# Kernel optimization log

Measured on AMD Instinct MI355X. Metric: run time of the kernel, lower is better.

The kernel has to match this reference:

```python
import jax, jax.numpy as jnp
import numpy as np

NUM_CLASSES = 80
SCORE_TH = 0.5
NMS_TH = 0.3
TOPK = 100          # per-class candidates kept before NMS
MAX_PER_IMAGE = 100
ANCHOR_MASK = [[6, 7, 8], [3, 4, 5], [0, 1, 2]]


def _decode_layer(f, anch, image_shape, input_shape):
    # f: [B, A*(5+C), gh, gw] -> boxes [B, gh*gw*A, 4], scores [B, gh*gw*A, C]
    B, _, gh, gw = f.shape
    A = anch.shape[0]
    f = f.reshape(B, A, NUM_CLASSES + 5, gh, gw).transpose(0, 3, 4, 1, 2)  # [B,gh,gw,A,5+C]
    gx = jnp.arange(gw, dtype=f.dtype)
    gy = jnp.arange(gh, dtype=f.dtype)
    X, Y = jnp.meshgrid(gx, gy, indexing='xy')            # each [gh,gw]
    grid = jnp.stack([X, Y], -1)[None, :, :, None, :]     # [1,gh,gw,1,2] (x,y)
    # faithful to original: divide (x,y) by tensor([gh,gw])
    box_xy = (jax.nn.sigmoid(f[..., :2]) + grid) / jnp.array([gh, gw], f.dtype)
    box_wh = jnp.exp(f[..., 2:4]) * anch[None, None, None, :, :] / input_shape
    conf = jax.nn.sigmoid(f[..., 4:5])
    probs = jax.nn.sigmoid(f[..., 5:])
    # yolo_correct_boxes (letterbox undo in normalized coords)
    box_yx = box_xy[..., ::-1]
    box_hw = box_wh[..., ::-1]
    new_shape = jnp.round(image_shape * jnp.min(input_shape / image_shape))
    offset = (input_shape - new_shape) / 2.0 / input_shape
    scale = input_shape / new_shape
    box_yx = (box_yx - offset) * scale
    box_hw = box_hw * scale
    mins = box_yx - box_hw / 2.0
    maxes = box_yx + box_hw / 2.0
    boxes = jnp.concatenate([mins, maxes], -1) * jnp.concatenate([image_shape, image_shape])
    return boxes.reshape(B, -1, 4), (conf * probs).reshape(B, -1, NUM_CLASSES)


def _pairwise_iou(b):  # b: [K,4] corner boxes
    area = jnp.maximum(b[:, 2] - b[:, 0], 0.0) * jnp.maximum(b[:, 3] - b[:, 1], 0.0)
    tl = jnp.maximum(b[:, None, :2], b[None, :, :2])
    br = jnp.minimum(b[:, None, 2:4], b[None, :, 2:4])
    wh = jnp.maximum(br - tl, 0.0)
    inter = wh[..., 0] * wh[..., 1]
    return inter / (area[:, None] + area[None, :] - inter + 1e-9)


def _detect(feats0, feats1, feats2, anchors, image_shape, ori_shape):
    input_shape = jnp.array([feats0.shape[2] * 32, feats0.shape[3] * 32], feats0.dtype)
    boxes_l, scores_l = [], []
    for l, f in enumerate([feats0, feats1, feats2]):
        b, s = _decode_layer(f, anchors[jnp.array(ANCHOR_MASK[l])], image_shape, input_shape)
        boxes_l.append(b)
        scores_l.append(s)
    boxes = jnp.concatenate(boxes_l, axis=1)    # [B,N,4]
    scores = jnp.concatenate(scores_l, axis=1)  # [B,N,C]

    def per_image(boxes_i, scores_i, ori_i):
        def per_class(sc):  # sc: [N]
            sc_m = jnp.where(sc >= SCORE_TH, sc, -1.0)
            vals, idx = jax.lax.top_k(sc_m, TOPK)      # sorted desc, like torch.sort
            b = boxes_i[idx]                            # [K,4]
            valid = vals >= SCORE_TH
            iou = _pairwise_iou(b)
            rng = jnp.arange(TOPK)
            def body(i, keep):
                sup = (iou[i] > NMS_TH) & (rng > i) & keep[i]
                return keep & ~sup
            keep = jax.lax.fori_loop(0, TOPK, body, valid)
            return b, vals, keep

        cand_b, cand_s, keep = jax.vmap(per_class, in_axes=1)(scores_i)  # [C,K,...]
        flat_s = jnp.where(keep, cand_s, -1.0).reshape(-1)               # [C*K]
        vals2, idx2 = jax.lax.top_k(flat_s, MAX_PER_IMAGE)
        det_boxes = cand_b.reshape(-1, 4)[idx2]                          # [M,4]
        det_valid = vals2 >= SCORE_TH
        det_cls = (idx2 // TOPK + 1).astype(jnp.int32)                   # classes shifted by +1
        # undo letterbox back to original image coords (per yolo_eval tail)
        w, h = image_shape[0], image_shape[1]
        iw, ih = ori_i[0], ori_i[1]
        scale = jnp.minimum(w / iw, h / ih)
        nw = jnp.floor(iw * scale)
        nh = jnp.floor(ih * scale)
        dx = jnp.floor((w - nw) / 2.0)
        dy = jnp.floor((h - nh) / 2.0)
        b02 = (det_boxes[:, jnp.array([0, 2])] - dx) / scale
        b13 = (det_boxes[:, jnp.array([1, 3])] - dy) / scale
        resc = jnp.stack([b02[:, 0], b13[:, 0], b02[:, 1], b13[:, 1]], -1)
        dets = jnp.concatenate([resc, vals2[:, None]], -1)               # [M,5]
        dets = jnp.where(det_valid[:, None], dets, 0.0)
        det_cls = jnp.where(det_valid, det_cls, 0)
        return dets, det_cls, det_valid

    return jax.vmap(per_image)(boxes, scores, ori_shape)


def setup_inputs() -> dict:
    key = jax.random.key(0)
    k0, k1, k2, k3 = jax.random.split(key, 4)
    B = 8
    feats0 = jax.random.normal(k0, (B, 255, 19, 19), jnp.float32)
    feats1 = jax.random.normal(k1, (B, 255, 38, 38), jnp.float32)
    feats2 = jax.random.normal(k2, (B, 255, 76, 76), jnp.float32)
    anchors = jnp.array([[10, 13], [16, 30], [33, 23], [30, 61], [62, 45],
                         [59, 119], [116, 90], [156, 198], [373, 326]], jnp.float32)
    image_shape = jnp.array([608.0, 608.0], jnp.float32)
    ori_shape = jax.random.randint(k3, (B, 2), 480, 1280).astype(jnp.float32)
    return {"feats0": feats0, "feats1": feats1, "feats2": feats2,
            "anchors": anchors, "image_shape": image_shape, "ori_shape": ori_shape}


def reference(feats0, feats1, feats2, anchors, image_shape, ori_shape):
    # Returns padded detections: dets [B,100,5] (ymin,xmin,ymax,xmax,score),
    # classes [B,100] int32 (0 = padding), valid [B,100] bool.
    return _detect(feats0, feats1, feats2, anchors, image_shape, ori_shape)
```

## Files before the change

kernel.cpp:

```cpp
#include <hip/hip_runtime.h>
#include <hip/hip_bf16.h>


#define BATCH 8
#define NC 80
#define G0 19
#define G1 38
#define G2 76
#define C0 (G0*G0)
#define C1 (G1*G1)
#define C2 (G2*G2)
#define CELLS (C0+C1+C2)
#define PCELLS 7616
#define OFF_L0 0
#define OFF_L1 (C0*3)
#define OFF_L2 (OFF_L1 + C1*3)
#define NBOX (CELLS*3)
#define TK 100
#define SCORE_TH 0.5f
#define NMS_TH 0.3f

#define CPG 10
#define NCG (NC/CPG)
#define SBLK 448
#define CHUNKS (PCELLS/SBLK)
#define SUBS 8
#define CAPS 512
#define CAP (SUBS*CAPS)

#define OFF_CAND   ((size_t)0)
#define OFF_BOXES  ((size_t)20971520)
#define OFF_CSCORE ((size_t)23882624)
#define OFF_CBOX   ((size_t)24138624)
#define OFF_STAGE  ((size_t)25162624)
#define OFF_CNT    ((size_t)25226624)

__device__ __forceinline__ float sigmoidf_(float x) {
    return 1.0f / (1.0f + expf(-x));
}

__device__ __forceinline__ void bitonic_desc(unsigned long long* s, unsigned M,
                                             unsigned tid, unsigned nthr) {
    for (unsigned k = 2; k <= M; k <<= 1) {
        for (unsigned j = k >> 1; j > 0; j >>= 1) {
            for (unsigned t = tid; t < M; t += nthr) {
                unsigned p = t ^ j;
                if (p > t) {
                    unsigned long long a = s[t], b = s[p];
                    bool desc = ((t & k) == 0);
                    if (desc ? (a < b) : (a > b)) { s[t] = b; s[p] = a; }
                }
            }
            __syncthreads();
        }
    }
}

__device__ __forceinline__ void cell_decomp(int cell, int& g, int& cl, int& off, int& layer) {
    if (cell < C0)            { layer = 0; g = G0; cl = cell;            off = OFF_L0; }
    else if (cell < C0 + C1)  { layer = 1; g = G1; cl = cell - C0;       off = OFF_L1; }
    else                      { layer = 2; g = G2; cl = cell - C0 - C1;  off = OFF_L2; }
}

__global__ __launch_bounds__(256) void box_kernel(
        const float* __restrict__ f0, const float* __restrict__ f1,
        const float* __restrict__ f2, const float* __restrict__ anchors,
        const float* __restrict__ image_shape,
        float* __restrict__ boxes) {
    int t = blockIdx.x * blockDim.x + threadIdx.x;
    if (t >= BATCH * NBOX) return;
    int b = t / NBOX;
    int r = t - b * NBOX;
    int a = r % 3;
    int cell = r / 3;

    int layer, g, cl, off;
    cell_decomp(cell, g, cl, off, layer);
    const float* f;
    if (layer == 0)      f = f0 + (size_t)b * 255 * C0;
    else if (layer == 1) f = f1 + (size_t)b * 255 * C1;
    else                 f = f2 + (size_t)b * 255 * C2;
    int S = g * g;
    int y = cl / g;
    int x = cl - y * g;

    const float in0 = (float)(G0 * 32);
    const float in1 = (float)(G0 * 32);
    float img0 = image_shape[0], img1 = image_shape[1];
    float mr   = fminf(in0 / img0, in1 / img1);
    float new0 = rintf(img0 * mr), new1 = rintf(img1 * mr);
    float ofs0 = (in0 - new0) * 0.5f / in0;
    float ofs1 = (in1 - new1) * 0.5f / in1;
    float scl0 = in0 / new0, scl1 = in1 / new1;

    const float* fa = f + (size_t)(a * 85) * S + cl;
    float tx = fa[0];
    float ty = fa[(size_t)S];
    float tw = fa[(size_t)2 * S];
    float th = fa[(size_t)3 * S];

    int am = (2 - layer) * 3 + a;
    float aw = anchors[am * 2 + 0];
    float ah = anchors[am * 2 + 1];

    float bx = (sigmoidf_(tx) + (float)x) / (float)g;
    float by = (sigmoidf_(ty) + (float)y) / (float)g;
    float bw = expf(tw) * aw / in0;
    float bh = expf(th) * ah / in1;

    float yy = (by - ofs0) * scl0;
    float xx = (bx - ofs1) * scl1;
    float hh = bh * scl0;
    float ww = bw * scl1;

    float4 bb;
    bb.x = (yy - hh * 0.5f) * img0;
    bb.y = (xx - ww * 0.5f) * img1;
    bb.z = (yy + hh * 0.5f) * img0;
    bb.w = (xx + ww * 0.5f) * img1;

    *(float4*)(boxes + ((size_t)b * NBOX + r) * 4) = bb;
}

__global__ __launch_bounds__(SBLK) void score_kernel(
        const float* __restrict__ f0, const float* __restrict__ f1,
        const float* __restrict__ f2,
        unsigned* __restrict__ cnt,
        unsigned long long* __restrict__ cand) {
    int chunk = blockIdx.x;
    int pg = blockIdx.y;
    int cgrp = pg % NCG;
    int a    = (pg / NCG) % 3;
    int b    = pg / (NCG * 3);

    int cellp = chunk * SBLK + threadIdx.x;
    int sub = (chunk * 7 + (threadIdx.x >> 6)) & (SUBS - 1);
    bool vc = (cellp < CELLS);
    int cell = vc ? cellp : 0;

    int layer, g, cl, off;
    cell_decomp(cell, g, cl, off, layer);
    const float* f;
    if (layer == 0)      f = f0 + (size_t)b * 255 * C0;
    else if (layer == 1) f = f1 + (size_t)b * 255 * C1;
    else                 f = f2 + (size_t)b * 255 * C2;
    int S = g * g;
    const float* fa = f + (size_t)(a * 85) * S + cl;

    float tc = vc ? fa[(size_t)4 * S] : -1e30f;
    float conf = sigmoidf_(tc);
    int gidx = off + cl * 3 + a;
    int lane = threadIdx.x & 63;

    float pl[CPG];
    #pragma unroll
    for (int k = 0; k < CPG; ++k) {
        int c = cgrp * CPG + k;
        pl[k] = vc ? fa[(size_t)(5 + c) * S] : -1e30f;
    }

    float sc[CPG];
    bool pred[CPG];
    #pragma unroll
    for (int k = 0; k < CPG; ++k) {
        sc[k] = conf * sigmoidf_(pl[k]);
        pred[k] = vc && (sc[k] >= SCORE_TH);
    }

    #pragma unroll
    for (int k = 0; k < CPG; ++k) {
        unsigned long long m = __ballot(pred[k]);
        if (m) {
            int c = cgrp * CPG + k;
            int idx = (b * NC + c) * SUBS + sub;
            int leader = __ffsll((long long)m) - 1;
            unsigned base = 0;
            if (lane == leader) base = atomicAdd(&cnt[idx], (unsigned)__popcll(m));
            base = (unsigned)__shfl((int)base, leader);
            if (pred[k]) {
                unsigned rank = (unsigned)__popcll(m & ((1ULL << lane) - 1ULL));
                unsigned slot = base + rank;
                if (slot < CAPS) {
                    unsigned long long key =
                        ((unsigned long long)__float_as_uint(sc[k]) << 32) |
                        (unsigned)(~(unsigned)gidx);
                    cand[(size_t)idx * CAPS + slot] = key;
                }
            }
        }
    }
}

__global__ __launch_bounds__(512) void nms_kernel(
        const unsigned* __restrict__ cnt,
        const unsigned long long* __restrict__ cand,
        const float* __restrict__ boxes,
        float* __restrict__ cscore, float* __restrict__ cbox) {
    __shared__ unsigned long long s[CAP];
    __shared__ float bx[TK][4];
    __shared__ float sc[TK];
    __shared__ int keep[TK];

    int bc = blockIdx.x;
    int b = bc / NC;
    unsigned tid = threadIdx.x;

    unsigned nI[SUBS];
    unsigned pref[SUBS + 1];
    pref[0] = 0;
    #pragma unroll
    for (int i = 0; i < SUBS; ++i) {
        unsigned v = cnt[bc * SUBS + i];
        nI[i] = v > CAPS ? CAPS : v;
        pref[i + 1] = pref[i] + nI[i];
    }
    unsigned n = pref[SUBS];
    unsigned M = 128;
    while (M < n) M <<= 1;

    for (unsigned t = tid; t < M; t += 512) s[t] = 0ULL;
    __syncthreads();
    #pragma unroll
    for (int i = 0; i < SUBS; ++i) {
        const unsigned long long* cp = cand + (size_t)(bc * SUBS + i) * CAPS;
        for (unsigned t = tid; t < nI[i]; t += 512) s[pref[i] + t] = cp[t];
    }
    __syncthreads();

    bitonic_desc(s, M, tid, 512);

    int nv = (int)n < TK ? (int)n : TK;
    if (tid < TK) {
        if ((int)tid < nv) {
            unsigned long long key = s[tid];
            sc[tid] = __uint_as_float((unsigned)(key >> 32));
            unsigned gidx = ~(unsigned)(key & 0xFFFFFFFFu);
            const float* bp = boxes + ((size_t)b * NBOX + gidx) * 4;
            bx[tid][0] = bp[0]; bx[tid][1] = bp[1];
            bx[tid][2] = bp[2]; bx[tid][3] = bp[3];
            keep[tid] = 1;
        } else {
            sc[tid] = -1.0f;
            bx[tid][0] = bx[tid][1] = bx[tid][2] = bx[tid][3] = 0.0f;
            keep[tid] = 0;
        }
    }
    __syncthreads();

    for (int i = 0; i < nv - 1; ++i) {
        bool ki = (keep[i] != 0);
        if (ki && (int)tid > i && (int)tid < nv && keep[tid]) {
            float a0 = bx[i][0], a1 = bx[i][1], a2 = bx[i][2], a3 = bx[i][3];
            float c0 = bx[tid][0], c1 = bx[tid][1], c2 = bx[tid][2], c3 = bx[tid][3];
            float areaA = fmaxf(a2 - a0, 0.0f) * fmaxf(a3 - a1, 0.0f);
            float areaC = fmaxf(c2 - c0, 0.0f) * fmaxf(c3 - c1, 0.0f);
            float tl0 = fmaxf(a0, c0), tl1 = fmaxf(a1, c1);
            float br0 = fminf(a2, c2), br1 = fminf(a3, c3);
            float w = fmaxf(br0 - tl0, 0.0f), h = fmaxf(br1 - tl1, 0.0f);
            float inter = w * h;
            float iou = inter / (areaA + areaC - inter + 1e-9f);
            if (iou > NMS_TH) keep[tid] = 0;
        }
        __syncthreads();
    }

    if (tid < TK) {
        int c = bc - b * NC;
        size_t o = (size_t)b * 8000 + (size_t)c * TK + tid;
        bool k = (keep[tid] != 0);
        cscore[o] = k ? sc[tid] : -1.0f;
        float* cb = cbox + o * 4;
        cb[0] = bx[tid][0]; cb[1] = bx[tid][1];
        cb[2] = bx[tid][2]; cb[3] = bx[tid][3];
    }
}

__device__ __forceinline__ unsigned fflip(float v) {
    unsigned u = __float_as_uint(v);
    return (u & 0x80000000u) ? ~u : (u | 0x80000000u);
}
__device__ __forceinline__ float funflip(unsigned u) {
    return __uint_as_float((u & 0x80000000u) ? (u & 0x7FFFFFFFu) : ~u);
}

__global__ __launch_bounds__(256) void topk1_kernel(
        const float* __restrict__ cscore, unsigned long long* __restrict__ stage) {
    __shared__ unsigned long long s[1024];
    int blk = blockIdx.x;
    int b = blk / 10;
    int g = blk - b * 10;
    unsigned tid = threadIdx.x;
    for (unsigned t = tid; t < 1024; t += 256) {
        unsigned long long key = 0ULL;
        if (t < 800) {
            unsigned e = (unsigned)(g * 800 + t);
            float v = cscore[(size_t)b * 8000 + e];
            key = ((unsigned long long)fflip(v) << 32) | (unsigned)(~e);
        }
        s[t] = key;
    }
    __syncthreads();
    bitonic_desc(s, 1024, tid, 256);
    if (tid < TK) stage[(size_t)b * 1000 + (size_t)g * TK + tid] = s[tid];
}

__global__ __launch_bounds__(256) void topk2_kernel(
        const unsigned long long* __restrict__ stage,
        const float* __restrict__ cbox,
        const float* __restrict__ image_shape,
        const float* __restrict__ ori,
        float* __restrict__ out) {
    __shared__ unsigned long long s[1024];
    int b = blockIdx.x;
    unsigned tid = threadIdx.x;
    for (unsigned t = tid; t < 1024; t += 256)
        s[t] = (t < 1000) ? stage[(size_t)b * 1000 + t] : 0ULL;
    __syncthreads();
    bitonic_desc(s, 1024, tid, 256);

    if (tid < TK) {
        unsigned long long key = s[tid];
        float v = funflip((unsigned)(key >> 32));
        unsigned e = ~(unsigned)(key & 0xFFFFFFFFu);
        bool valid = (v >= SCORE_TH);

        float w = image_shape[0], h = image_shape[1];
        float iw = ori[b * 2 + 0], ih = ori[b * 2 + 1];
        float scale = fminf(w / iw, h / ih);
        float nw = floorf(iw * scale), nh = floorf(ih * scale);
        float dx = floorf((w - nw) * 0.5f), dy = floorf((h - nh) * 0.5f);

        const float* cb = cbox + ((size_t)b * 8000 + e) * 4;
        float r0 = (cb[0] - dx) / scale;
        float r1 = (cb[1] - dy) / scale;
        float r2 = (cb[2] - dx) / scale;
        float r3 = (cb[3] - dy) / scale;

        size_t row = (size_t)b * TK + tid;
        float* dp = out + row * 5;
        dp[0] = valid ? r0 : 0.0f;
        dp[1] = valid ? r1 : 0.0f;
        dp[2] = valid ? r2 : 0.0f;
        dp[3] = valid ? r3 : 0.0f;
        dp[4] = valid ? v  : 0.0f;
        out[(size_t)BATCH * TK * 5 + row] = valid ? (float)(e / TK + 1) : 0.0f;
        out[(size_t)BATCH * TK * 6 + row] = valid ? 1.0f : 0.0f;
    }
}

extern "C" void kernel_launch(void* const* d_in, const int* in_sizes, int n_in,
                              void* d_out, int out_size, void* d_ws, size_t ws_size,
                              hipStream_t stream) {
    const float* f0  = (const float*)d_in[0];
    const float* f1  = (const float*)d_in[1];
    const float* f2  = (const float*)d_in[2];
    const float* anc = (const float*)d_in[3];
    const float* ish = (const float*)d_in[4];
    const float* ori = (const float*)d_in[5];
    float* out = (float*)d_out;

    char* ws = (char*)d_ws;
    unsigned long long* cand  = (unsigned long long*)(ws + OFF_CAND);
    float*              boxes = (float*)(ws + OFF_BOXES);
    float*              cscr  = (float*)(ws + OFF_CSCORE);
    float*              cbox  = (float*)(ws + OFF_CBOX);
    unsigned long long* stage = (unsigned long long*)(ws + OFF_STAGE);
    unsigned*           cnt   = (unsigned*)(ws + OFF_CNT);

    hipMemsetAsync(cnt, 0, BATCH * NC * SUBS * sizeof(unsigned), stream);

    {
        int nThreads = BATCH * NBOX;
        int nBlocks = (nThreads + 255) / 256;
        box_kernel<<<nBlocks, 256, 0, stream>>>(f0, f1, f2, anc, ish, boxes);
    }

    {
        dim3 grid(CHUNKS, BATCH * 3 * NCG);
        score_kernel<<<grid, SBLK, 0, stream>>>(f0, f1, f2, cnt, cand);
    }

    nms_kernel<<<BATCH * NC, 512, 0, stream>>>(cnt, cand, boxes, cscr, cbox);

    topk1_kernel<<<BATCH * 10, 256, 0, stream>>>(cscr, stage);

    topk2_kernel<<<BATCH, 256, 0, stream>>>(stage, cbox, ish, ori, out);
}
```

Baseline: 331.8 us.

## Replace shared-memory bitonic sort and NMS with wavefront-shuffle top-k merge and NMS

The per-class NMS kernel now sorts 128-element chunks inside each wavefront with shuffle-based bitonic networks, then merges chunks pairwise keeping only the top 128, instead of a full block-wide bitonic sort with a barrier per step. The greedy NMS loop runs in a single wavefront, holding boxes and keep bits in registers and broadcasting by shuffle, which removes the per-iteration __syncthreads. It also uses float4 box loads and stores and halves the block size. The risks are extra shuffle instructions for 64-bit keys and a serial NMS loop on one wavefront while the other waves sit idle.

```diff
diff --git a/kernel.cpp b/kernel.cpp
--- a/kernel.cpp
+++ b/kernel.cpp
@@ -60,6 +60,56 @@
     if (cell < C0)            { layer = 0; g = G0; cl = cell;            off = OFF_L0; }
     else if (cell < C0 + C1)  { layer = 1; g = G1; cl = cell - C0;       off = OFF_L1; }
     else                      { layer = 2; g = G2; cl = cell - C0 - C1;  off = OFF_L2; }
+}
+
+__device__ __forceinline__ unsigned long long maxu(unsigned long long a, unsigned long long b) { return a > b ? a : b; }
+__device__ __forceinline__ unsigned long long minu(unsigned long long a, unsigned long long b) { return a < b ? a : b; }
+
+__device__ __forceinline__ unsigned long long ux64(unsigned long long v, int m) {
+    int lo = __shfl_xor((int)(unsigned)v, m, 64);
+    int hi = __shfl_xor((int)(unsigned)(v >> 32), m, 64);
+    return ((unsigned long long)(unsigned)hi << 32) | (unsigned)lo;
+}
+
+__device__ __forceinline__ void wsort128(unsigned long long& v0, unsigned long long& v1, int lane) {
+    #pragma unroll
+    for (int k = 2; k <= 32; k <<= 1) {
+        #pragma unroll
+        for (int j = k >> 1; j >= 1; j >>= 1) {
+            bool desc = ((lane & k) == 0);
+            bool lower = ((lane & j) == 0);
+            bool km = (lower == desc);
+            unsigned long long p0 = ux64(v0, j); v0 = km ? maxu(v0, p0) : minu(v0, p0);
+            unsigned long long p1 = ux64(v1, j); v1 = km ? maxu(v1, p1) : minu(v1, p1);
+        }
+    }
+    #pragma unroll
+    for (int j = 32; j >= 1; j >>= 1) {
+        bool lower = ((lane & j) == 0);
+        unsigned long long p0 = ux64(v0, j); v0 = lower ? maxu(v0, p0) : minu(v0, p0);
+        unsigned long long p1 = ux64(v1, j); v1 = lower ? minu(v1, p1) : maxu(v1, p1);
+    }
+    { unsigned long long t0 = maxu(v0, v1), t1 = minu(v0, v1); v0 = t0; v1 = t1; }
+    #pragma unroll
+    for (int j = 32; j >= 1; j >>= 1) {
+        bool lower = ((lane & j) == 0);
+        unsigned long long p0 = ux64(v0, j); v0 = lower ? maxu(v0, p0) : minu(v0, p0);
+        unsigned long long p1 = ux64(v1, j); v1 = lower ? maxu(v1, p1) : minu(v1, p1);
+    }
+}
+
+__device__ __forceinline__ void wmergetop(unsigned long long& a0, unsigned long long& a1,
+                                          unsigned long long b0, unsigned long long b1, int lane) {
+    unsigned long long r0 = ux64(b1, 63);
+    unsigned long long r1 = ux64(b0, 63);
+    a0 = maxu(a0, r0); a1 = maxu(a1, r1);
+    { unsigned long long t0 = maxu(a0, a1), t1 = minu(a0, a1); a0 = t0; a1 = t1; }
+    #pragma unroll
+    for (int j = 32; j >= 1; j >>= 1) {
+        bool lower = ((lane & j) == 0);
+        unsigned long long p0 = ux64(a0, j); a0 = lower ? maxu(a0, p0) : minu(a0, p0);
+        unsigned long long p1 = ux64(a1, j); a1 = lower ? maxu(a1, p1) : minu(a1, p1);
+    }
 }
 
 __global__ __launch_bounds__(256) void box_kernel(
@@ -191,87 +241,120 @@
     }
 }
 
-__global__ __launch_bounds__(512) void nms_kernel(
+__global__ __launch_bounds__(256) void nms_kernel(
         const unsigned* __restrict__ cnt,
         const unsigned long long* __restrict__ cand,
         const float* __restrict__ boxes,
         float* __restrict__ cscore, float* __restrict__ cbox) {
-    __shared__ unsigned long long s[CAP];
-    __shared__ float bx[TK][4];
-    __shared__ float sc[TK];
-    __shared__ int keep[TK];
+    __shared__ unsigned long long s[SUBS * CAPS];
 
     int bc = blockIdx.x;
     int b = bc / NC;
-    unsigned tid = threadIdx.x;
-
-    unsigned nI[SUBS];
+    int c = bc - b * NC;
+    int tid = threadIdx.x;
+    int lane = tid & 63;
+    int wid = tid >> 6;
+
     unsigned pref[SUBS + 1];
     pref[0] = 0;
     #pragma unroll
     for (int i = 0; i < SUBS; ++i) {
         unsigned v = cnt[bc * SUBS + i];
-        nI[i] = v > CAPS ? CAPS : v;
-        pref[i + 1] = pref[i] + nI[i];
+        v = v > CAPS ? CAPS : v;
+        pref[i + 1] = pref[i] + v;
     }
     unsigned n = pref[SUBS];
-    unsigned M = 128;
-    while (M < n) M <<= 1;
-
-    for (unsigned t = tid; t < M; t += 512) s[t] = 0ULL;
+    int nchunks = (int)((n + 127u) >> 7);
+    int P = 1;
+    while (P < nchunks) P <<= 1;
+
+    const unsigned long long* cbase = cand + (size_t)bc * (SUBS * CAPS);
+
+    for (int ch = wid; ch < P; ch += 4) {
+        unsigned e0 = (unsigned)(ch * 128 + lane);
+        unsigned e1 = e0 + 64;
+        unsigned long long v0 = 0ULL, v1 = 0ULL;
+        if (e0 < n) {
+            unsigned adj = 0;
+            #pragma unroll
+            for (int q = 1; q < SUBS; ++q) if (e0 >= pref[q]) adj = (unsigned)(q * CAPS) - pref[q];
+            v0 = cbase[e0 + adj];
+        }
+        if (e1 < n) {
+            unsigned adj = 0;
+            #pragma unroll
+            for (int q = 1; q < SUBS; ++q) if (e1 >= pref[q]) adj = (unsigned)(q * CAPS) - pref[q];
+            v1 = cbase[e1 + adj];
+        }
+        wsort128(v0, v1, lane);
+        s[ch * 128 + lane] = v0;
+        s[ch * 128 + 64 + lane] = v1;
+    }
     __syncthreads();
-    #pragma unroll
-    for (int i = 0; i < SUBS; ++i) {
-        const unsigned long long* cp = cand + (size_t)(bc * SUBS + i) * CAPS;
-        for (unsigned t = tid; t < nI[i]; t += 512) s[pref[i] + t] = cp[t];
-    }
-    __syncthreads();
-
-    bitonic_desc(s, M, tid, 512);
-
-    int nv = (int)n < TK ? (int)n : TK;
-    if (tid < TK) {
-        if ((int)tid < nv) {
-            unsigned long long key = s[tid];
-            sc[tid] = __uint_as_float((unsigned)(key >> 32));
-            unsigned gidx = ~(unsigned)(key & 0xFFFFFFFFu);
-            const float* bp = boxes + ((size_t)b * NBOX + gidx) * 4;
-            bx[tid][0] = bp[0]; bx[tid][1] = bp[1];
-            bx[tid][2] = bp[2]; bx[tid][3] = bp[3];
-            keep[tid] = 1;
-        } else {
-            sc[tid] = -1.0f;
-            bx[tid][0] = bx[tid][1] = bx[tid][2] = bx[tid][3] = 0.0f;
-            keep[tid] = 0;
-        }
-    }
-    __syncthreads();
-
-    for (int i = 0; i < nv - 1; ++i) {
-        bool ki = (keep[i] != 0);
-        if (ki && (int)tid > i && (int)tid < nv && keep[tid]) {
-            float a0 = bx[i][0], a1 = bx[i][1], a2 = bx[i][2], a3 = bx[i][3];
-            float c0 = bx[tid][0], c1 = bx[tid][1], c2 = bx[tid][2], c3 = bx[tid][3];
-            float areaA = fmaxf(a2 - a0, 0.0f) * fmaxf(a3 - a1, 0.0f);
-            float areaC = fmaxf(c2 - c0, 0.0f) * fmaxf(c3 - c1, 0.0f);
-            float tl0 = fmaxf(a0, c0), tl1 = fmaxf(a1, c1);
-            float br0 = fminf(a2, c2), br1 = fminf(a3, c3);
-            float w = fmaxf(br0 - tl0, 0.0f), h = fmaxf(br1 - tl1, 0.0f);
-            float inter = w * h;
-            float iou = inter / (areaA + areaC - inter + 1e-9f);
-            if (iou > NMS_TH) keep[tid] = 0;
+
+    for (int S2 = P >> 1; S2 >= 1; S2 >>= 1) {
+        for (int m = wid; m < S2; m += 4) {
+            unsigned long long a0 = s[m * 128 + lane], a1 = s[m * 128 + 64 + lane];
+            unsigned long long b0 = s[(m + S2) * 128 + lane], b1 = s[(m + S2) * 128 + 64 + lane];
+            wmergetop(a0, a1, b0, b1, lane);
+            s[m * 128 + lane] = a0;
+            s[m * 128 + 64 + lane] = a1;
         }
         __syncthreads();
     }
 
-    if (tid < TK) {
-        int c = bc - b * NC;
-        size_t o = (size_t)b * 8000 + (size_t)c * TK + tid;
-        bool k = (keep[tid] != 0);
-        cscore[o] = k ? sc[tid] : -1.0f;
-        float* cb = cbox + o * 4;
-        cb[0] = bx[tid][0]; cb[1] = bx[tid][1];
-        cb[2] = bx[tid][2]; cb[3] = bx[tid][3];
+    if (wid == 0) {
+        int nv = (int)n < TK ? (int)n : TK;
+        unsigned long long k0 = s[lane], k1 = s[64 + lane];
+        int e0 = lane, e1 = 64 + lane;
+        bool val0 = e0 < nv, val1 = e1 < nv;
+        float sc0 = __uint_as_float((unsigned)(k0 >> 32));
+        float sc1 = __uint_as_float((unsigned)(k1 >> 32));
+        unsigned g0 = ~(unsigned)(k0 & 0xFFFFFFFFu);
+        unsigned g1 = ~(unsigned)(k1 & 0xFFFFFFFFu);
+        float4 B0 = make_float4(0.f, 0.f, 0.f, 0.f);
+        float4 B1 = make_float4(0.f, 0.f, 0.f, 0.f);
+        if (val0) B0 = *(const float4*)(boxes + ((size_t)b * NBOX + g0) * 4);
+        if (val1) B1 = *(const float4*)(boxes + ((size_t)b * NBOX + g1) * 4);
+        unsigned keepw = (val0 ? 1u : 0u) | (val1 ? 2u : 0u);
+
+        for (int i = 0; i + 1 < nv; ++i) {
+            unsigned kw = (unsigned)__shfl((int)keepw, i & 63);
+            if (!((kw >> (i >> 6)) & 1u)) continue;
+            float ax = __shfl((i < 64) ? B0.x : B1.x, i & 63);
+            float ay = __shfl((i < 64) ? B0.y : B1.y, i & 63);
+            float az = __shfl((i < 64) ? B0.z : B1.z, i & 63);
+            float aw = __shfl((i < 64) ? B0.w : B1.w, i & 63);
+            float areaA = fmaxf(az - ax, 0.0f) * fmaxf(aw - ay, 0.0f);
+            if ((keepw & 1u) && e0 > i) {
+                float areaC = fmaxf(B0.z - B0.x, 0.0f) * fmaxf(B0.w - B0.y, 0.0f);
+                float tl0 = fmaxf(ax, B0.x), tl1 = fmaxf(ay, B0.y);
+                float br0 = fminf(az, B0.z), br1 = fminf(aw, B0.w);
+                float w = fmaxf(br0 - tl0, 0.0f), h = fmaxf(br1 - tl1, 0.0f);
+                float inter = w * h;
+                float iou = inter / (areaA + areaC - inter + 1e-9f);
+                if (iou > NMS_TH) keepw &= ~1u;
+            }
+            if ((keepw & 2u) && e1 > i) {
+                float areaC = fmaxf(B1.z - B1.x, 0.0f) * fmaxf(B1.w - B1.y, 0.0f);
+                float tl0 = fmaxf(ax, B1.x), tl1 = fmaxf(ay, B1.y);
+                float br0 = fminf(az, B1.z), br1 = fminf(aw, B1.w);
+                float w = fmaxf(br0 - tl0, 0.0f), h = fmaxf(br1 - tl1, 0.0f);
+                float inter = w * h;
+                float iou = inter / (areaA + areaC - inter + 1e-9f);
+                if (iou > NMS_TH) keepw &= ~2u;
+            }
+        }
+
+        size_t obase = (size_t)b * 8000 + (size_t)c * TK;
+        if (e0 < TK) {
+            cscore[obase + e0] = (keepw & 1u) ? sc0 : -1.0f;
+            *(float4*)(cbox + (obase + e0) * 4) = B0;
+        }
+        if (e1 < TK) {
+            cscore[obase + e1] = (keepw & 2u) ? sc1 : -1.0f;
+            *(float4*)(cbox + (obase + e1) * 4) = B1;
+        }
     }
 }
 
@@ -380,7 +463,7 @@
         score_kernel<<<grid, SBLK, 0, stream>>>(f0, f1, f2, cnt, cand);
     }
 
-    nms_kernel<<<BATCH * NC, 512, 0, stream>>>(cnt, cand, boxes, cscr, cbox);
+    nms_kernel<<<BATCH * NC, 256, 0, stream>>>(cnt, cand, boxes, cscr, cbox);
 
     topk1_kernel<<<BATCH * 10, 256, 0, stream>>>(cscr, stage);
 
```

After: 288.2 us. -13.1%, faster.
